# Kernel tuning notes

Hardware: AMD Instinct MI355X
Metric: run time of the kernel (lower is better)

The kernel has to match this reference:

```python
import jax, jax.numpy as jnp
import numpy as np

TOP_K = 2  # args.num_experts_per_tok


def setup_inputs() -> dict:
    key = jax.random.key(0)
    k1, k2, k3 = jax.random.split(key, 3)
    B, S, H, O, E = 8192, 1, 4096, 4096, 8
    x = jax.random.normal(k1, (B, S, H), dtype=jnp.float32)
    gate_w = jax.random.normal(k2, (H, E), dtype=jnp.float32) * 0.02
    expert_w = jax.random.normal(k3, (E, H, O), dtype=jnp.float32) * 0.02
    return {"x": x, "gate_w": gate_w, "expert_w": expert_w}


def reference(x, gate_w, expert_w):
    # x: [B, S, H]; gate_w: [H, E]; expert_w: [E, H, O]
    E = gate_w.shape[-1]
    # Gating matmul (gate_logits_BS8 in the original)
    logits = jnp.einsum("bsh,he->bse", x, gate_w)
    # top-k expert selection, then softmax over the k selected logits
    topv, topi = jax.lax.top_k(logits, TOP_K)          # [B, S, K]
    w = jax.nn.softmax(topv, axis=-1)                   # [B, S, K]
    # Scatter top-k weights into a dense per-expert weight map.
    # Equivalent to the per-device boolean-mask gather (batch_ids/head_pos)
    # + weighted scatter + cross-device sum in the original.
    onehot = jax.nn.one_hot(topi, E, dtype=x.dtype)     # [B, S, K, E]
    w_e = jnp.einsum("bske,bsk->bse", onehot, w)        # [B, S, E]
    # Weighted combine of per-expert outputs: out = sum_e w_e * (x @ W_e)
    out = jnp.einsum("bsh,eho,bse->bso", x, expert_w, w_e)
    return out
```

## Files before the change

kernel.cpp:

```cpp
#include <hip/hip_runtime.h>
#include <cstdint>
#include <cstddef>

#define TOKENS 8192
#define HDIM 4096
#define ODIM 4096
#define NEXP 8

using short8  = __attribute__((ext_vector_type(8))) short;
using floatx4 = __attribute__((ext_vector_type(4))) float;

__device__ __forceinline__ unsigned short f2bf(float f) {
  unsigned u = __float_as_uint(f);
  u = u + 0x7fffu + ((u >> 16) & 1u);
  return (unsigned short)(u >> 16);
}

__device__ __forceinline__ void async_ld16(const void* g, void* l) {
  __builtin_amdgcn_global_load_lds((const __attribute__((address_space(1))) void*)g,
                                   (__attribute__((address_space(3))) void*)l,
                                   16, 0, 0);
}

__global__ __launch_bounds__(256) void gate_kernel(
    const float* __restrict__ x, const float* __restrict__ gw,
    unsigned short* __restrict__ xb, int* __restrict__ counts,
    int* __restrict__ lists, float* __restrict__ wts)
{
  const int b = blockIdx.x;
  const int t = threadIdx.x;
  const float4* xr = (const float4*)(x + (size_t)b * HDIM);

  double acc[NEXP];
#pragma unroll
  for (int e = 0; e < NEXP; ++e) acc[e] = 0.0;

#pragma unroll
  for (int i = 0; i < 4; ++i) {
    const int idx = i * 256 + t;
    const float4 v = xr[idx];
    ushort4 pack = make_ushort4(f2bf(v.x), f2bf(v.y), f2bf(v.z), f2bf(v.w));
    *(ushort4*)(xb + (size_t)b * HDIM + (size_t)idx * 4) = pack;
    const float* g = gw + (size_t)idx * 4 * NEXP;
    const float xs[4] = {v.x, v.y, v.z, v.w};
#pragma unroll
    for (int j = 0; j < 4; ++j) {
      const float4 g0 = *(const float4*)(g + j * NEXP);
      const float4 g1 = *(const float4*)(g + j * NEXP + 4);
      const double xv = (double)xs[j];
      acc[0] += xv * (double)g0.x; acc[1] += xv * (double)g0.y;
      acc[2] += xv * (double)g0.z; acc[3] += xv * (double)g0.w;
      acc[4] += xv * (double)g1.x; acc[5] += xv * (double)g1.y;
      acc[6] += xv * (double)g1.z; acc[7] += xv * (double)g1.w;
    }
  }

#pragma unroll
  for (int off = 32; off > 0; off >>= 1)
#pragma unroll
    for (int e = 0; e < NEXP; ++e)
      acc[e] += __shfl_down(acc[e], off);

  __shared__ double sred[4][NEXP];
  const int w = t >> 6, lane = t & 63;
  if (lane == 0)
#pragma unroll
    for (int e = 0; e < NEXP; ++e) sred[w][e] = acc[e];
  __syncthreads();

  if (t == 0) {
    double lg[NEXP];
#pragma unroll
    for (int e = 0; e < NEXP; ++e)
      lg[e] = sred[0][e] + sred[1][e] + sred[2][e] + sred[3][e];
    int i0 = 0; double v0 = lg[0];
    for (int e = 1; e < NEXP; ++e) if (lg[e] > v0) { v0 = lg[e]; i0 = e; }
    int i1 = -1; double v1 = -1e300;
    for (int e = 0; e < NEXP; ++e) if (e != i0 && lg[e] > v1) { v1 = lg[e]; i1 = e; }
    const double d = exp(v1 - v0);
    const float w0 = (float)(1.0 / (1.0 + d));
    const float w1 = (float)(d / (1.0 + d));
    wts[2 * b]     = w0;
    wts[2 * b + 1] = w1;
    int p0 = atomicAdd(&counts[i0], 1);
    lists[i0 * TOKENS + p0] = 2 * b;
    int p1 = atomicAdd(&counts[i1], 1);
    lists[i1 * TOKENS + p1] = 2 * b + 1;
  }
}

__global__ __launch_bounds__(256) void wt_kernel(
    const float* __restrict__ W, unsigned short* __restrict__ wt)
{
  const int e  = blockIdx.z;
  const int h0 = blockIdx.y * 64;
  const int o0 = blockIdx.x * 64;
  const int t  = threadIdx.x;
  __shared__ unsigned T[64 * 33];

  const float* Wb = W + (size_t)e * HDIM * ODIM;
  const int rp = t >> 4;
  const int cq = t & 15;
#pragma unroll
  for (int p = 0; p < 2; ++p) {
    const int h = 2 * rp + 32 * p;
    const float4 v0 = *(const float4*)(Wb + (size_t)(h0 + h) * ODIM + o0 + 4 * cq);
    const float4 v1 = *(const float4*)(Wb + (size_t)(h0 + h + 1) * ODIM + o0 + 4 * cq);
    const float a0[4] = {v0.x, v0.y, v0.z, v0.w};
    const float a1[4] = {v1.x, v1.y, v1.z, v1.w};
#pragma unroll
    for (int j = 0; j < 4; ++j) {
      unsigned d = (unsigned)f2bf(a0[j]) | ((unsigned)f2bf(a1[j]) << 16);
      T[(4 * cq + j) * 33 + (h >> 1)] = d;
    }
  }
  __syncthreads();

#pragma unroll
  for (int p = 0; p < 2; ++p) {
    const int o_l = p * 32 + (t >> 3);
    const int dw  = (t & 7) * 4;
    const unsigned d0 = T[o_l * 33 + dw];
    const unsigned d1 = T[o_l * 33 + dw + 1];
    const unsigned d2 = T[o_l * 33 + dw + 2];
    const unsigned d3 = T[o_l * 33 + dw + 3];
    uint4 pack = make_uint4(d0, d1, d2, d3);
    *(uint4*)(wt + ((size_t)e * ODIM + o0 + o_l) * HDIM + h0 + dw * 2) = pack;
  }
}

__global__ __launch_bounds__(256) void moe_gemm(
    const unsigned short* __restrict__ xb, const unsigned short* __restrict__ wt,
    const int* __restrict__ counts, const int* __restrict__ lists,
    const float* __restrict__ wts, float* __restrict__ out,
    float* __restrict__ ybuf, int mode)
{
  const int e   = blockIdx.z;
  const int cnt = counts[e];
  const int m0  = blockIdx.y * 128;
  if (m0 >= cnt) return;
  const int n0  = blockIdx.x * 128;

  __shared__ unsigned short As[128 * 64];
  __shared__ unsigned short Bs[128 * 64];
  __shared__ int   rid[128];
  __shared__ float rw[128];

  const int t    = threadIdx.x;
  const int w    = t >> 6;
  const int lane = t & 63;

  if (t < 128) {
    const int r  = m0 + t;
    const int cr = (r < cnt) ? r : (cnt - 1);
    const int sid = lists[e * TOKENS + cr];
    rid[t] = sid;
    rw[t]  = (r < cnt) ? wts[sid] : 0.0f;
  }
  __syncthreads();

  const int sub  = lane >> 3;
  const int csw  = ((lane & 7) ^ sub) * 8;
  const unsigned short* aSrc[4];
  const unsigned short* bSrc[4];
#pragma unroll
  for (int i = 0; i < 4; ++i) {
    const int rr = i * 32 + w * 8 + sub;
    aSrc[i] = xb + (size_t)(rid[rr] >> 1) * HDIM + csw;
    bSrc[i] = wt + ((size_t)e * ODIM + n0 + rr) * HDIM + csw;
  }

  floatx4 acc[4][4];
#pragma unroll
  for (int i = 0; i < 4; ++i)
#pragma unroll
    for (int j = 0; j < 4; ++j)
      acc[i][j] = (floatx4){0.f, 0.f, 0.f, 0.f};

  const int wm   = (w >> 1) * 64;
  const int wn   = (w & 1) * 64;
  const int frow = lane & 15;
  const int fk   = lane >> 4;
  const int rsw  = frow & 7;

  for (int kt = 0; kt < HDIM / 64; ++kt) {
#pragma unroll
    for (int i = 0; i < 4; ++i) {
      async_ld16(aSrc[i], As + (i * 32 + w * 8) * 64);
      async_ld16(bSrc[i], Bs + (i * 32 + w * 8) * 64);
      aSrc[i] += 64; bSrc[i] += 64;
    }
    __syncthreads();
#pragma unroll
    for (int kk = 0; kk < 2; ++kk) {
      short8 af[4], bfr[4];
#pragma unroll
      for (int mt = 0; mt < 4; ++mt)
        af[mt] = *(const short8*)(As + (wm + mt * 16 + frow) * 64 +
                                  (((kk * 4 + fk) ^ rsw) * 8));
#pragma unroll
      for (int nt = 0; nt < 4; ++nt)
        bfr[nt] = *(const short8*)(Bs + (wn + nt * 16 + frow) * 64 +
                                   (((kk * 4 + fk) ^ rsw) * 8));
#pragma unroll
      for (int mt = 0; mt < 4; ++mt)
#pragma unroll
        for (int nt = 0; nt < 4; ++nt)
          acc[mt][nt] = __builtin_amdgcn_mfma_f32_16x16x32_bf16(af[mt], bfr[nt], acc[mt][nt], 0, 0, 0);
    }
    __syncthreads();
  }

#pragma unroll
  for (int mt = 0; mt < 4; ++mt) {
    const int lrb = wm + mt * 16 + (lane >> 4) * 4;
#pragma unroll
    for (int r = 0; r < 4; ++r) {
      const int lr = lrb + r;
      if (m0 + lr < cnt) {
        const float wgt = rw[lr];
        if (mode) {
          float* ob = ybuf + (size_t)rid[lr] * ODIM + n0 + wn + (lane & 15);
#pragma unroll
          for (int nt = 0; nt < 4; ++nt)
            ob[nt * 16] = wgt * acc[mt][nt][r];
        } else {
          float* ob = out + (size_t)(rid[lr] >> 1) * ODIM + n0 + wn + (lane & 15);
#pragma unroll
          for (int nt = 0; nt < 4; ++nt)
            atomicAdd(ob + nt * 16, wgt * acc[mt][nt][r]);
        }
      }
    }
  }
}

__global__ __launch_bounds__(256) void combine_kernel(
    const float* __restrict__ ybuf, float* __restrict__ out)
{
  const int b = blockIdx.x;
  const int t = threadIdx.x;
  const float4* y0 = (const float4*)(ybuf + (size_t)(2 * b) * ODIM);
  const float4* y1 = (const float4*)(ybuf + (size_t)(2 * b + 1) * ODIM);
  float4* o = (float4*)(out + (size_t)b * ODIM);
#pragma unroll
  for (int i = 0; i < 4; ++i) {
    const int idx = i * 256 + t;
    const float4 a = y0[idx];
    const float4 c = y1[idx];
    o[idx] = make_float4(a.x + c.x, a.y + c.y, a.z + c.z, a.w + c.w);
  }
}

extern "C" void kernel_launch(void* const* d_in, const int* in_sizes, int n_in,
                              void* d_out, int out_size, void* d_ws, size_t ws_size,
                              hipStream_t stream) {
  const float* x  = (const float*)d_in[0];
  const float* gw = (const float*)d_in[1];
  const float* ew = (const float*)d_in[2];
  float* out = (float*)d_out;

  char* ws = (char*)d_ws;
  unsigned short* wt = (unsigned short*)ws;
  size_t off = (size_t)NEXP * HDIM * ODIM * 2;
  unsigned short* xb = (unsigned short*)(ws + off);
  off += (size_t)TOKENS * HDIM * 2;
  int*   counts = (int*)(ws + off); off += 128;
  int*   lists  = (int*)(ws + off); off += (size_t)NEXP * TOKENS * sizeof(int);
  float* wts    = (float*)(ws + off); off += (size_t)TOKENS * 2 * sizeof(float);
  off = (off + 255) & ~(size_t)255;
  float* ybuf   = (float*)(ws + off);
  const size_t need = off + (size_t)TOKENS * 2 * ODIM * sizeof(float);
  const int fast = (ws_size >= need) ? 1 : 0;
  (void)in_sizes; (void)n_in;

  hipMemsetAsync(counts, 0, 128, stream);
  if (!fast)
    hipMemsetAsync(d_out, 0, (size_t)out_size * sizeof(float), stream);

  gate_kernel<<<TOKENS, 256, 0, stream>>>(x, gw, xb, counts, lists, wts);
  wt_kernel<<<dim3(ODIM / 64, HDIM / 64, NEXP), 256, 0, stream>>>(ew, wt);
  moe_gemm<<<dim3(ODIM / 128, TOKENS / 128, NEXP), 256, 0, stream>>>(
      xb, wt, counts, lists, wts, out, ybuf, fast);
  if (fast)
    combine_kernel<<<TOKENS, 256, 0, stream>>>(ybuf, out);
}
```

Baseline: 1.817 ms.

## Double-buffer LDS tiles in MoE GEMM to overlap global loads with MFMA

Splits the shared-memory A/B tiles into two buffers and restructures the K loop so the next tile's async global-to-LDS loads are issued before computing on the current tile. A manual vmcnt(8) wait lets the in-flight loads for the next stage stay outstanding while the current stage is consumed. Scheduling barriers keep the compiler from reordering across the stages. This doubles LDS usage per block, which may reduce occupancy, and depends on the vmcnt accounting matching the 8 loads issued per stage.

```diff
diff --git a/kernel.cpp b/kernel.cpp
--- a/kernel.cpp
+++ b/kernel.cpp
@@ -21,6 +21,9 @@
                                    (__attribute__((address_space(3))) void*)l,
                                    16, 0, 0);
 }
+
+__device__ __forceinline__ void wait_vm8() { asm volatile("s_waitcnt vmcnt(8)" ::: "memory"); }
+__device__ __forceinline__ void wait_vm0() { asm volatile("s_waitcnt vmcnt(0)" ::: "memory"); }
 
 __global__ __launch_bounds__(256) void gate_kernel(
     const float* __restrict__ x, const float* __restrict__ gw,
@@ -141,8 +144,10 @@
   if (m0 >= cnt) return;
   const int n0  = blockIdx.x * 128;
 
-  __shared__ unsigned short As[128 * 64];
-  __shared__ unsigned short Bs[128 * 64];
+  __shared__ unsigned short As0[128 * 64];
+  __shared__ unsigned short As1[128 * 64];
+  __shared__ unsigned short Bs0[128 * 64];
+  __shared__ unsigned short Bs1[128 * 64];
   __shared__ int   rid[128];
   __shared__ float rw[128];
 
@@ -183,24 +188,26 @@
   const int fk   = lane >> 4;
   const int rsw  = frow & 7;
 
-  for (int kt = 0; kt < HDIM / 64; ++kt) {
+  auto STAGE = [&](unsigned short* A, unsigned short* B) {
 #pragma unroll
     for (int i = 0; i < 4; ++i) {
-      async_ld16(aSrc[i], As + (i * 32 + w * 8) * 64);
-      async_ld16(bSrc[i], Bs + (i * 32 + w * 8) * 64);
+      async_ld16(aSrc[i], A + (i * 32 + w * 8) * 64);
+      async_ld16(bSrc[i], B + (i * 32 + w * 8) * 64);
       aSrc[i] += 64; bSrc[i] += 64;
     }
-    __syncthreads();
+  };
+
+  auto COMPUTE = [&](const unsigned short* A, const unsigned short* B) {
 #pragma unroll
     for (int kk = 0; kk < 2; ++kk) {
       short8 af[4], bfr[4];
 #pragma unroll
       for (int mt = 0; mt < 4; ++mt)
-        af[mt] = *(const short8*)(As + (wm + mt * 16 + frow) * 64 +
+        af[mt] = *(const short8*)(A + (wm + mt * 16 + frow) * 64 +
                                   (((kk * 4 + fk) ^ rsw) * 8));
 #pragma unroll
       for (int nt = 0; nt < 4; ++nt)
-        bfr[nt] = *(const short8*)(Bs + (wn + nt * 16 + frow) * 64 +
+        bfr[nt] = *(const short8*)(B + (wn + nt * 16 + frow) * 64 +
                                    (((kk * 4 + fk) ^ rsw) * 8));
 #pragma unroll
       for (int mt = 0; mt < 4; ++mt)
@@ -208,8 +215,38 @@
         for (int nt = 0; nt < 4; ++nt)
           acc[mt][nt] = __builtin_amdgcn_mfma_f32_16x16x32_bf16(af[mt], bfr[nt], acc[mt][nt], 0, 0, 0);
     }
-    __syncthreads();
-  }
+  };
+
+  STAGE(As0, Bs0);
+
+#pragma unroll 1
+  for (int kt2 = 0; kt2 < 31; ++kt2) {
+    STAGE(As1, Bs1);
+    wait_vm8();
+    __builtin_amdgcn_s_barrier();
+    __builtin_amdgcn_sched_barrier(0);
+    COMPUTE(As0, Bs0);
+    __builtin_amdgcn_sched_barrier(0);
+    __builtin_amdgcn_s_barrier();
+    STAGE(As0, Bs0);
+    wait_vm8();
+    __builtin_amdgcn_s_barrier();
+    __builtin_amdgcn_sched_barrier(0);
+    COMPUTE(As1, Bs1);
+    __builtin_amdgcn_sched_barrier(0);
+    __builtin_amdgcn_s_barrier();
+  }
+  STAGE(As1, Bs1);
+  wait_vm8();
+  __builtin_amdgcn_s_barrier();
+  __builtin_amdgcn_sched_barrier(0);
+  COMPUTE(As0, Bs0);
+  __builtin_amdgcn_sched_barrier(0);
+  __builtin_amdgcn_s_barrier();
+  wait_vm0();
+  __builtin_amdgcn_s_barrier();
+  __builtin_amdgcn_sched_barrier(0);
+  COMPUTE(As1, Bs1);
 
 #pragma unroll
   for (int mt = 0; mt < 4; ++mt) {
```

Result: faster. 1.720 ms (-5.3%).
